# Optimization experiments

Hardware: AMD Instinct MI355X
Metric: run time of the kernel (lower is better)

## Reference

```python
import jax, jax.numpy as jnp
import numpy as np

B, L, D, H, I = 4, 1024, 2048, 16, 8192
DH = D // H  # 128
EPS = 1e-6


def setup_inputs() -> dict:
    key = jax.random.key(0)
    ks = jax.random.split(key, 10)
    hidden_states = jax.random.normal(ks[0], (B, L, D), dtype=jnp.float32)
    # additive causal mask [B,1,L,L]: 0 on allowed, large negative on masked
    causal = jnp.tril(jnp.ones((L, L), dtype=bool))
    attention_mask = jnp.where(causal, 0.0, -1e9).astype(jnp.float32)
    attention_mask = jnp.broadcast_to(attention_mask[None, None], (B, 1, L, L))
    # RoPE tables [B,L,DH]
    inv_freq = 1.0 / (10000.0 ** (jnp.arange(0, DH, 2, dtype=jnp.float32) / DH))
    pos = jnp.arange(L, dtype=jnp.float32)
    freqs = pos[:, None] * inv_freq[None, :]            # [L, DH/2]
    emb = jnp.concatenate([freqs, freqs], axis=-1)       # [L, DH]
    cos = jnp.broadcast_to(jnp.cos(emb)[None], (B, L, DH)).astype(jnp.float32)
    sin = jnp.broadcast_to(jnp.sin(emb)[None], (B, L, DH)).astype(jnp.float32)
    s = 0.02
    return {
        "hidden_states": hidden_states,
        "attention_mask": attention_mask,
        "cos": cos,
        "sin": sin,
        "q_w": jax.random.normal(ks[1], (D, D), jnp.float32) * s,
        "k_w": jax.random.normal(ks[2], (D, D), jnp.float32) * s,
        "v_w": jax.random.normal(ks[3], (D, D), jnp.float32) * s,
        "o_w": jax.random.normal(ks[4], (D, D), jnp.float32) * s,
        "gate_w": jax.random.normal(ks[5], (I, D), jnp.float32) * s,
        "up_w": jax.random.normal(ks[6], (I, D), jnp.float32) * s,
        "down_w": jax.random.normal(ks[7], (D, I), jnp.float32) * s,
        "ln1_w": jnp.ones((D,), jnp.float32),
        "ln2_w": jnp.ones((D,), jnp.float32),
    }


def _rms_norm(x, w):
    var = jnp.mean(jnp.square(x), axis=-1, keepdims=True)
    return x * jax.lax.rsqrt(var + EPS) * w


def _rotate_half(x):
    x1, x2 = jnp.split(x, 2, axis=-1)
    return jnp.concatenate([-x2, x1], axis=-1)


def reference(hidden_states, attention_mask, cos, sin, q_w, k_w, v_w, o_w,
              gate_w, up_w, down_w, ln1_w, ln2_w):
    residual = hidden_states
    h = _rms_norm(hidden_states, ln1_w)                       # [B,L,D]
    # QKV projections (torch Linear: x @ W^T)
    def heads(x, w):
        return (x @ w.T).reshape(B, L, H, DH).transpose(0, 2, 1, 3)  # [B,H,L,DH]
    q, k, v = heads(h, q_w), heads(h, k_w), heads(h, v_w)
    cos_b, sin_b = cos[:, None], sin[:, None]                 # [B,1,L,DH]
    q = q * cos_b + _rotate_half(q) * sin_b
    k = k * cos_b + _rotate_half(k) * sin_b
    scores = jnp.einsum('bhqd,bhkd->bhqk', q, k) / jnp.sqrt(jnp.float32(DH))
    scores = scores + attention_mask                          # [B,H,L,L]
    attn = jax.nn.softmax(scores, axis=-1)
    ctx = jnp.einsum('bhqk,bhkd->bhqd', attn, v)              # [B,H,L,DH]
    ctx = ctx.transpose(0, 2, 1, 3).reshape(B, L, D)
    attn_out = ctx @ o_w.T
    h1 = residual + attn_out
    h2 = _rms_norm(h1, ln2_w)
    mlp = (jax.nn.silu(h2 @ gate_w.T) * (h2 @ up_w.T)) @ down_w.T
    out = h1 + mlp
    return out, attn
```

## Files before the change

kernel.cpp:

```cpp
#include <hip/hip_runtime.h>


typedef __bf16 bf16;
typedef __bf16 bf16x8 __attribute__((ext_vector_type(8)));
typedef __bf16 bf16x4 __attribute__((ext_vector_type(4)));
typedef float  f32x4  __attribute__((ext_vector_type(4)));

constexpr int   kB  = 4;
constexpr int   kL  = 1024;
constexpr int   kD  = 2048;
constexpr int   kH  = 16;
constexpr int   kI  = 8192;
constexpr int   kDH = 128;
constexpr int   kQKV = 3 * kD;
constexpr float kEps = 1e-6f;
constexpr float kScoreScale = 0.08838834764831845f;

typedef __attribute__((address_space(1))) void gvoid_t;
typedef __attribute__((address_space(3))) void lvoid_t;

__device__ __forceinline__ void gload_lds16(const void* g, void* l) {
  __builtin_amdgcn_global_load_lds((gvoid_t*)g, (lvoid_t*)l, 16, 0, 0);
}

#define ASM_VMCNT(n) asm volatile("s_waitcnt vmcnt(" #n ")" ::: "memory")

__device__ __forceinline__ void bar_raw() {
  asm volatile("" ::: "memory");
  __builtin_amdgcn_s_barrier();
  asm volatile("" ::: "memory");
}

__global__ __launch_bounds__(256) void cast_f32_bf16_kernel(
    const float* __restrict__ x, bf16* __restrict__ y, long n) {
  long i = ((long)blockIdx.x * 256 + threadIdx.x) * 4;
  long stride = (long)gridDim.x * 256 * 4;
  for (; i < n; i += stride) {
    const float4 v = *reinterpret_cast<const float4*>(x + i);
    bf16x4 o;
    o[0] = (bf16)v.x; o[1] = (bf16)v.y; o[2] = (bf16)v.z; o[3] = (bf16)v.w;
    *reinterpret_cast<bf16x4*>(y + i) = o;
  }
}

__global__ __launch_bounds__(256) void rmsnorm_kernel(
    const float* __restrict__ x, const float* __restrict__ w,
    bf16* __restrict__ out) {
  const long row = blockIdx.x;
  const float* xr = x + row * (long)kD;
  bf16* orow = out + row * (long)kD;
  const int t = threadIdx.x;

  float4 v0 = *(const float4*)(xr + t * 8);
  float4 v1 = *(const float4*)(xr + t * 8 + 4);
  float ss = v0.x * v0.x + v0.y * v0.y + v0.z * v0.z + v0.w * v0.w +
             v1.x * v1.x + v1.y * v1.y + v1.z * v1.z + v1.w * v1.w;

  __shared__ float red[4];
  for (int off = 32; off > 0; off >>= 1) ss += __shfl_down(ss, off);
  if ((t & 63) == 0) red[t >> 6] = ss;
  __syncthreads();
  const float tot = red[0] + red[1] + red[2] + red[3];
  const float rs = rsqrtf(tot / (float)kD + kEps);

  float4 w0 = *(const float4*)(w + t * 8);
  float4 w1 = *(const float4*)(w + t * 8 + 4);
  bf16x8 o;
  o[0] = (bf16)(v0.x * rs * w0.x); o[1] = (bf16)(v0.y * rs * w0.y);
  o[2] = (bf16)(v0.z * rs * w0.z); o[3] = (bf16)(v0.w * rs * w0.w);
  o[4] = (bf16)(v1.x * rs * w1.x); o[5] = (bf16)(v1.y * rs * w1.y);
  o[6] = (bf16)(v1.z * rs * w1.z); o[7] = (bf16)(v1.w * rs * w1.w);
  *(bf16x8*)(orow + t * 8) = o;
}

__global__ __launch_bounds__(256) void rope_kernel(
    bf16* __restrict__ qkv, const float* __restrict__ cosb,
    const float* __restrict__ sinb) {
  const long row = blockIdx.x;
  const float* cr = cosb + row * (long)kDH;
  const float* sr = sinb + row * (long)kDH;
  bf16* qr = qkv + row * (long)kQKV;
  bf16* kr = qr + kD;
  const int t = threadIdx.x;
#pragma unroll
  for (int it = 0; it < 4; ++it) {
    const int p = it * 256 + t;
    const int h = p >> 6, i = p & 63;
    const int i0 = h * kDH + i, i1 = i0 + 64;
    const float c0 = cr[i], s0 = sr[i], c1 = cr[i + 64], s1 = sr[i + 64];
    const float q0 = (float)qr[i0], q1 = (float)qr[i1];
    qr[i0] = (bf16)(q0 * c0 - q1 * s0);
    qr[i1] = (bf16)(q1 * c1 + q0 * s1);
    const float k0 = (float)kr[i0], k1 = (float)kr[i1];
    kr[i0] = (bf16)(k0 * c0 - k1 * s0);
    kr[i1] = (bf16)(k1 * c1 + k0 * s1);
  }
}

__global__ __launch_bounds__(256) void transpose_v_kernel(
    const bf16* __restrict__ qkv, bf16* __restrict__ vT) {
  __shared__ bf16 tile[32][33];
  const int z = blockIdx.z, b = z / kH, h = z % kH;
  const bf16* src = qkv + (long)b * kL * kQKV + 2 * kD + h * kDH;
  bf16* dst = vT + (long)z * kDH * kL;
  const int l0 = blockIdx.x * 32, d0 = blockIdx.y * 32;
  const int tx = threadIdx.x & 31, ty = threadIdx.x >> 5;
  for (int r = ty; r < 32; r += 8)
    tile[r][tx] = src[(long)(l0 + r) * kQKV + d0 + tx];
  __syncthreads();
  for (int r = ty; r < 32; r += 8)
    dst[(long)(d0 + r) * kL + l0 + tx] = tile[tx][r];
}

__global__ __launch_bounds__(256) void merge_stats_kernel(
    const float2* __restrict__ sp, float2* __restrict__ sm) {
  const int idx = blockIdx.x * 256 + threadIdx.x;
  const int row = idx & 1023;
  const int n = ((row >> 7) + 1) * 2;
  const float2* p = sp + ((long)idx << 4);
  float M = -3.0e38f;
  for (int i = 0; i < n; ++i) M = fmaxf(M, p[i].x);
  float S = 0.f;
  for (int i = 0; i < n; ++i) S += p[i].y * expf(p[i].x - M);
  sm[idx] = make_float2(M, 1.0f / S);
}

enum { EPI_NONE = 0, EPI_ADD = 1, EPI_SILU = 3, EPI_OUTADD = 4,
       EPI_PASS1 = 6, EPI_PASS2 = 7 };

template <typename OutT, int EPI, bool AF32, int NF, bool CK>
__device__ __forceinline__ void gemm_body(
    const void* __restrict__ Ap, long sAo, long sAi, int lda,
    const bf16* __restrict__ Bp, long sBo, long sBi, int ldb,
    OutT* Cp, long sCo, long sCi, int ldc,
    const void* Ep, long sEo, long sEi, int lde,
    float scale, int Hdiv, int M, int N, int K) {
  constexpr int BN = 32 * NF;
  constexpr int ACH = 512;
  constexpr int BCH = BN * 4;
  static_assert((EPI != EPI_PASS1 && EPI != EPI_PASS2) || NF == 4, "pass NF=4");

  const int z = blockIdx.z;
  const int zo = z / Hdiv, zi = z % Hdiv;

  const bf16* A = nullptr;
  const float* Af = nullptr;
  if constexpr (AF32) Af = (const float*)Ap + zo * sAo + zi * sAi;
  else                A  = (const bf16*)Ap + zo * sAo + zi * sAi;
  const bf16* Bw = Bp + zo * sBo + zi * sBi;
  OutT* C = Cp + zo * sCo + zi * sCi;

  const int t = threadIdx.x;
  const int m0 = blockIdx.y * 128, n0 = blockIdx.x * BN;

  if constexpr (EPI == EPI_PASS1) {
    if (blockIdx.x > blockIdx.y) return;
  }
  if constexpr (EPI == EPI_PASS2) {
    if (blockIdx.x > blockIdx.y) {
      for (int e = t; e < 128 * 32; e += 256) {
        const int row = e >> 5, col = (e & 31) * 4;
        *(float4*)&C[(long)(m0 + row) * ldc + n0 + col] =
            make_float4(0.f, 0.f, 0.f, 0.f);
      }
      return;
    }
  }

  __shared__ __align__(16) bf16 lsA[2][128 * 32];
  __shared__ __align__(16) bf16 lsB[2][BN * 32];

  const int wave = t >> 6, lane = t & 63;
  const int wm = (wave >> 1) * 64, wn = (wave & 1) * (NF * 16);
  const int lr = lane & 15, lg = lane >> 4;

  f32x4 acc[4][NF] = {};

  auto stage = [&](int buf, int k0) {
    if constexpr (AF32) {
#pragma unroll
      for (int c = 0; c < 2; ++c) {
        const int id = c * 256 + t;
        const int row = id >> 2, col = (id & 3) * 8;
        const float* src = Af + (long)(m0 + row) * lda + k0 + col;
        const float4 u0 = *(const float4*)src;
        const float4 u1 = *(const float4*)(src + 4);
        bf16x8 wv;
        wv[0] = (bf16)u0.x; wv[1] = (bf16)u0.y; wv[2] = (bf16)u0.z; wv[3] = (bf16)u0.w;
        wv[4] = (bf16)u1.x; wv[5] = (bf16)u1.y; wv[6] = (bf16)u1.z; wv[7] = (bf16)u1.w;
        *(bf16x8*)&lsA[buf][id * 8] = wv;
        if (NF == 4 || c == 0)
          gload_lds16(Bw + (long)(n0 + row) * ldb + k0 + col, &lsB[buf][id * 8]);
      }
    } else {
#pragma unroll
      for (int c = 0; c < (ACH + BCH) / 256; ++c) {
        const int id = c * 256 + t;
        if (id < ACH) {
          const int row = id >> 2, col = (id & 3) * 8;
          gload_lds16(A + (long)(m0 + row) * lda + k0 + col, &lsA[buf][id * 8]);
        } else {
          const int fid = id - ACH;
          const int row = fid >> 2, col = (fid & 3) * 8;
          gload_lds16(Bw + (long)(n0 + row) * ldb + k0 + col, &lsB[buf][fid * 8]);
        }
      }
    }
  };

  auto compute = [&](int buf) {
    bf16x8 af[4], bfr[NF];
#pragma unroll
    for (int i = 0; i < 4; ++i)
      af[i] = *(const bf16x8*)&lsA[buf][(wm + i * 16 + lr) * 32 + lg * 8];
#pragma unroll
    for (int j = 0; j < NF; ++j)
      bfr[j] = *(const bf16x8*)&lsB[buf][(wn + j * 16 + lr) * 32 + lg * 8];
#pragma unroll
    for (int i = 0; i < 4; ++i)
#pragma unroll
      for (int j = 0; j < NF; ++j)
        acc[i][j] = __builtin_amdgcn_mfma_f32_16x16x32_bf16(af[i], bfr[j],
                                                            acc[i][j], 0, 0, 0);
  };

  const int Klim = CK ? (m0 + 128) : K;
  int cur = 0;

  if constexpr (AF32) {
    stage(0, 0);
    __syncthreads();
    for (int k0 = 0; k0 < Klim - 32; k0 += 32) {
      stage(cur ^ 1, k0 + 32);
      compute(cur);
      __syncthreads();
      cur ^= 1;
    }
    compute(cur);
  } else {
    stage(0, 0);
    for (int k0 = 0; k0 < Klim - 32; k0 += 32) {
      stage(cur ^ 1, k0 + 32);
      if constexpr (NF == 4) ASM_VMCNT(4); else ASM_VMCNT(3);
      bar_raw();
      compute(cur);
      bar_raw();
      cur ^= 1;
    }
    ASM_VMCNT(0);
    bar_raw();
    compute(cur);
  }

  if constexpr (EPI == EPI_PASS1) {
    float2* statsP = (float2*)Ep;
    const int half = wn >> 6, nt = blockIdx.x;
#pragma unroll
    for (int i = 0; i < 4; ++i) {
#pragma unroll
      for (int r = 0; r < 4; ++r) {
        const int rowg = m0 + wm + i * 16 + lg * 4 + r;
        float v[NF];
        float mx = -3.0e38f;
#pragma unroll
        for (int j = 0; j < NF; ++j) {
          const int colg = n0 + wn + j * 16 + lr;
          v[j] = acc[i][j][r] * scale + (colg > rowg ? -1.0e9f : 0.0f);
          mx = fmaxf(mx, v[j]);
        }
        for (int sh = 1; sh <= 8; sh <<= 1) mx = fmaxf(mx, __shfl_xor(mx, sh));
        float s = 0.f;
#pragma unroll
        for (int j = 0; j < NF; ++j) s += expf(v[j] - mx);
        for (int sh = 1; sh <= 8; sh <<= 1) s += __shfl_xor(s, sh);
        if (lr == 0)
          statsP[(((long)(z << 10) + rowg) << 4) + nt * 2 + half] =
              make_float2(mx, s);
      }
    }
  } else if constexpr (EPI == EPI_PASS2) {
    const float2* sm = (const float2*)Ep;
#pragma unroll
    for (int i = 0; i < 4; ++i) {
#pragma unroll
      for (int j = 0; j < NF; ++j) {
        const int colg = n0 + wn + j * 16 + lr;
#pragma unroll
        for (int r = 0; r < 4; ++r) {
          const int rowg = m0 + wm + i * 16 + lg * 4 + r;
          float p = 0.0f;
          if (colg <= rowg) {
            const float2 st = sm[(z << 10) + rowg];
            p = expf(acc[i][j][r] * scale - st.x) * st.y;
          }
          C[(long)rowg * ldc + colg] = (OutT)p;
        }
      }
    }
  } else {
    const float* Ef = (const float*)Ep;
    const bf16* Eb = (const bf16*)Ep;
    long ebase = 0;
    if constexpr (EPI == EPI_ADD || EPI == EPI_SILU)
      ebase = zo * sEo + zi * sEi;
#pragma unroll
    for (int i = 0; i < 4; ++i) {
#pragma unroll
      for (int j = 0; j < NF; ++j) {
        const int col = n0 + wn + j * 16 + lr;
#pragma unroll
        for (int r = 0; r < 4; ++r) {
          const int rowi = m0 + wm + i * 16 + lg * 4 + r;
          float val = acc[i][j][r] * scale;
          const long idx = (long)rowi * ldc + col;
          if constexpr (EPI == EPI_ADD)
            val += Ef[ebase + (long)rowi * lde + col];
          if constexpr (EPI == EPI_SILU) {
            const float g = (float)Eb[ebase + (long)rowi * lde + col];
            val = (g / (1.0f + expf(-g))) * val;
          }
          if constexpr (EPI == EPI_OUTADD)
            val += (float)C[idx];
          C[idx] = (OutT)val;
        }
      }
    }
  }
}

#define GEMM_ARGS                                                        \
  const void* __restrict__ Ap, long sAo, long sAi, int lda,              \
  const bf16* __restrict__ Bp, long sBo, long sBi, int ldb,              \
  void* Cp, long sCo, long sCi, int ldc,                                 \
  const void* Ep, long sEo, long sEi, int lde,                           \
  float scale, int Hdiv, int M, int N, int K
#define GEMM_PASS Ap, sAo, sAi, lda, Bp, sBo, sBi, ldb, (OUT_T*)Cp, sCo, \
  sCi, ldc, Ep, sEo, sEi, lde, scale, Hdiv, M, N, K

#define DEF_GEMM(NAME, OUT_TY, EPI_V, AF32_V, NF_V, CK_V)                \
  __global__ __launch_bounds__(256) void NAME(GEMM_ARGS) {               \
    using OUT_T = OUT_TY;                                                \
    gemm_body<OUT_T, EPI_V, AF32_V, NF_V, CK_V>(GEMM_PASS);              \
  }

DEF_GEMM(gemm_qkv,   bf16,  EPI_NONE,   false, 4, false)
DEF_GEMM(gemm_sc1,   float, EPI_PASS1,  false, 4, false)
DEF_GEMM(gemm_sc2,   float, EPI_PASS2,  false, 4, false)
DEF_GEMM(gemm_ctx,   bf16,  EPI_NONE,   true,  2, true)
DEF_GEMM(gemm_oproj, float, EPI_ADD,    false, 2, false)
DEF_GEMM(gemm_gate,  bf16,  EPI_NONE,   false, 4, false)
DEF_GEMM(gemm_up,    bf16,  EPI_SILU,   false, 4, false)
DEF_GEMM(gemm_down,  float, EPI_OUTADD, false, 2, false)

extern "C" void kernel_launch(void* const* d_in, const int* in_sizes, int n_in,
                              void* d_out, int out_size, void* d_ws,
                              size_t ws_size, hipStream_t stream) {
  (void)in_sizes; (void)n_in; (void)out_size; (void)ws_size;

  const float* hidden = (const float*)d_in[0];
  const float* cosb   = (const float*)d_in[2];
  const float* sinb   = (const float*)d_in[3];
  const float* q_w    = (const float*)d_in[4];
  const float* k_w    = (const float*)d_in[5];
  const float* v_w    = (const float*)d_in[6];
  const float* o_w    = (const float*)d_in[7];
  const float* gate_w = (const float*)d_in[8];
  const float* up_w   = (const float*)d_in[9];
  const float* down_w = (const float*)d_in[10];
  const float* ln1    = (const float*)d_in[11];
  const float* ln2    = (const float*)d_in[12];

  float* out  = (float*)d_out;
  float* attn = out + (long)kB * kL * kD;

  bf16* wsb = (bf16*)d_ws;
  long off = 0;
  bf16* WQKV = wsb + off; off += 3L * kD * kD;
  bf16* WO   = wsb + off; off += (long)kD * kD;
  bf16* WBIG = wsb + off; off += (long)kI * kD;
  bf16* HBF  = wsb + off; off += (long)kB * kL * kD;
  bf16* QKV  = wsb + off; off += (long)kB * kL * kQKV;
  bf16* GBUF = wsb + off; off += (long)kB * kL * kI;

  float2* STATS_P = (float2*)HBF;
  float2* STATS_M = STATS_P + (64L * 1024 * 16);

  const long DD = (long)kD * kD;
  const long ID = (long)kI * kD;
  const int  ML = kB * kL;

  cast_f32_bf16_kernel<<<dim3((int)(DD / 1024)), 256, 0, stream>>>(q_w, WQKV, DD);
  cast_f32_bf16_kernel<<<dim3((int)(DD / 1024)), 256, 0, stream>>>(k_w, WQKV + DD, DD);
  cast_f32_bf16_kernel<<<dim3((int)(DD / 1024)), 256, 0, stream>>>(v_w, WQKV + 2 * DD, DD);
  cast_f32_bf16_kernel<<<dim3((int)(DD / 1024)), 256, 0, stream>>>(o_w, WO, DD);

  rmsnorm_kernel<<<ML, 256, 0, stream>>>(hidden, ln1, HBF);

  gemm_qkv<<<dim3(kQKV / 128, ML / 128, 1), 256, 0, stream>>>(
      HBF, 0, 0, kD, WQKV, 0, 0, kD, QKV, 0, 0, kQKV,
      nullptr, 0, 0, 0, 1.0f, 1, ML, kQKV, kD);

  rope_kernel<<<ML, 256, 0, stream>>>(QKV, cosb, sinb);

  transpose_v_kernel<<<dim3(kL / 32, kDH / 32, kB * kH), 256, 0, stream>>>(QKV, GBUF);

  gemm_sc1<<<dim3(kL / 128, kL / 128, kB * kH), 256, 0, stream>>>(
      QKV, (long)kL * kQKV, kDH, kQKV,
      QKV + kD, (long)kL * kQKV, kDH, kQKV,
      attn, (long)kH * kL * kL, (long)kL * kL, kL,
      STATS_P, 0, 0, 0,
      kScoreScale, kH, kL, kL, kDH);

  merge_stats_kernel<<<256, 256, 0, stream>>>(STATS_P, STATS_M);

  gemm_sc2<<<dim3(kL / 128, kL / 128, kB * kH), 256, 0, stream>>>(
      QKV, (long)kL * kQKV, kDH, kQKV,
      QKV + kD, (long)kL * kQKV, kDH, kQKV,
      attn, (long)kH * kL * kL, (long)kL * kL, kL,
      STATS_M, 0, 0, 0,
      kScoreScale, kH, kL, kL, kDH);

  gemm_ctx<<<dim3(kDH / 64, kL / 128, kB * kH), 256, 0, stream>>>(
      attn, (long)kH * kL * kL, (long)kL * kL, kL,
      GBUF, (long)kH * kDH * kL, (long)kDH * kL, kL,
      HBF, (long)kL * kD, kDH, kD,
      nullptr, 0, 0, 0, 1.0f, kH, kL, kDH, kL);

  gemm_oproj<<<dim3(kD / 64, ML / 128, 1), 256, 0, stream>>>(
      HBF, 0, 0, kD, WO, 0, 0, kD, out, 0, 0, kD,
      hidden, 0, 0, kD, 1.0f, 1, ML, kD, kD);

  bf16* H2 = QKV;
  rmsnorm_kernel<<<ML, 256, 0, stream>>>(out, ln2, H2);

  cast_f32_bf16_kernel<<<dim3((int)(ID / 1024)), 256, 0, stream>>>(gate_w, WBIG, ID);
  gemm_gate<<<dim3(kI / 128, ML / 128, 1), 256, 0, stream>>>(
      H2, 0, 0, kD, WBIG, 0, 0, kD, GBUF, 0, 0, kI,
      nullptr, 0, 0, 0, 1.0f, 1, ML, kI, kD);

  cast_f32_bf16_kernel<<<dim3((int)(ID / 1024)), 256, 0, stream>>>(up_w, WBIG, ID);
  gemm_up<<<dim3(kI / 128, ML / 128, 1), 256, 0, stream>>>(
      H2, 0, 0, kD, WBIG, 0, 0, kD, GBUF, 0, 0, kI,
      GBUF, 0, 0, kI, 1.0f, 1, ML, kI, kD);

  cast_f32_bf16_kernel<<<dim3((int)(ID / 1024)), 256, 0, stream>>>(down_w, WBIG, ID);
  gemm_down<<<dim3(kD / 64, ML / 128, 1), 256, 0, stream>>>(
      GBUF, 0, 0, kI, WBIG, 0, 0, kI, out, 0, 0, kD,
      nullptr, 0, 0, 0, 1.0f, 1, ML, kD, kI);
}
```

Baseline: 1.153 ms.

## Fuse gate/up GEMMs with SiLU, add XCD block swizzle, simplify pipeline sync

Replaces the separate gate and up GEMMs (gate writes bf16 to GBUF, up rereads it for the SiLU epilogue) with one gemm_mlp kernel. It loads the activation tile once, computes both gate and up accumulators, and applies SiLU*up in registers, removing an intermediate round trip. It also adds an XCD-aware block index remap for the qkv, oproj and down GEMMs to improve L2 locality. Separately, it drops the hand-tuned vmcnt/raw-barrier pipeline for bf16 inputs in favour of plain __syncthreads, which may reduce load/compute overlap. It needs an extra 8192x2048 bf16 weight buffer in workspace.

```diff
diff --git a/kernel.cpp b/kernel.cpp
--- a/kernel.cpp
+++ b/kernel.cpp
@@ -21,14 +21,6 @@
 
 __device__ __forceinline__ void gload_lds16(const void* g, void* l) {
   __builtin_amdgcn_global_load_lds((gvoid_t*)g, (lvoid_t*)l, 16, 0, 0);
-}
-
-#define ASM_VMCNT(n) asm volatile("s_waitcnt vmcnt(" #n ")" ::: "memory")
-
-__device__ __forceinline__ void bar_raw() {
-  asm volatile("" ::: "memory");
-  __builtin_amdgcn_s_barrier();
-  asm volatile("" ::: "memory");
 }
 
 __global__ __launch_bounds__(256) void cast_f32_bf16_kernel(
@@ -125,10 +117,9 @@
   sm[idx] = make_float2(M, 1.0f / S);
 }
 
-enum { EPI_NONE = 0, EPI_ADD = 1, EPI_SILU = 3, EPI_OUTADD = 4,
-       EPI_PASS1 = 6, EPI_PASS2 = 7 };
-
-template <typename OutT, int EPI, bool AF32, int NF, bool CK>
+enum { EPI_NONE = 0, EPI_ADD = 1, EPI_OUTADD = 4, EPI_PASS1 = 6, EPI_PASS2 = 7 };
+
+template <typename OutT, int EPI, bool AF32, int NF, bool CK, bool SWZ>
 __device__ __forceinline__ void gemm_body(
     const void* __restrict__ Ap, long sAo, long sAi, int lda,
     const bf16* __restrict__ Bp, long sBo, long sBi, int ldb,
@@ -151,7 +142,16 @@
   OutT* C = Cp + zo * sCo + zi * sCi;
 
   const int t = threadIdx.x;
-  const int m0 = blockIdx.y * 128, n0 = blockIdx.x * BN;
+
+  int bx = blockIdx.x, by = blockIdx.y;
+  if constexpr (SWZ) {
+    const int nn = gridDim.x, nm = gridDim.y;
+    const int f = by * nn + bx;
+    const int xcd = f & 7, j = f >> 3;
+    by = j % nm;
+    bx = xcd * (nn >> 3) + j / nm;
+  }
+  const int m0 = by * 128, n0 = bx * BN;
 
   if constexpr (EPI == EPI_PASS1) {
     if (blockIdx.x > blockIdx.y) return;
@@ -225,32 +225,17 @@
   };
 
   const int Klim = CK ? (m0 + 128) : K;
+
+  stage(0, 0);
+  __syncthreads();
   int cur = 0;
-
-  if constexpr (AF32) {
-    stage(0, 0);
+  for (int k0 = 0; k0 < Klim - 32; k0 += 32) {
+    stage(cur ^ 1, k0 + 32);
+    compute(cur);
     __syncthreads();
-    for (int k0 = 0; k0 < Klim - 32; k0 += 32) {
-      stage(cur ^ 1, k0 + 32);
-      compute(cur);
-      __syncthreads();
-      cur ^= 1;
-    }
-    compute(cur);
-  } else {
-    stage(0, 0);
-    for (int k0 = 0; k0 < Klim - 32; k0 += 32) {
-      stage(cur ^ 1, k0 + 32);
-      if constexpr (NF == 4) ASM_VMCNT(4); else ASM_VMCNT(3);
-      bar_raw();
-      compute(cur);
-      bar_raw();
-      cur ^= 1;
-    }
-    ASM_VMCNT(0);
-    bar_raw();
-    compute(cur);
-  }
+    cur ^= 1;
+  }
+  compute(cur);
 
   if constexpr (EPI == EPI_PASS1) {
     float2* statsP = (float2*)Ep;
@@ -299,9 +284,8 @@
     }
   } else {
     const float* Ef = (const float*)Ep;
-    const bf16* Eb = (const bf16*)Ep;
     long ebase = 0;
-    if constexpr (EPI == EPI_ADD || EPI == EPI_SILU)
+    if constexpr (EPI == EPI_ADD)
       ebase = zo * sEo + zi * sEi;
 #pragma unroll
     for (int i = 0; i < 4; ++i) {
@@ -315,10 +299,6 @@
           const long idx = (long)rowi * ldc + col;
           if constexpr (EPI == EPI_ADD)
             val += Ef[ebase + (long)rowi * lde + col];
-          if constexpr (EPI == EPI_SILU) {
-            const float g = (float)Eb[ebase + (long)rowi * lde + col];
-            val = (g / (1.0f + expf(-g))) * val;
-          }
           if constexpr (EPI == EPI_OUTADD)
             val += (float)C[idx];
           C[idx] = (OutT)val;
@@ -337,20 +317,99 @@
 #define GEMM_PASS Ap, sAo, sAi, lda, Bp, sBo, sBi, ldb, (OUT_T*)Cp, sCo, \
   sCi, ldc, Ep, sEo, sEi, lde, scale, Hdiv, M, N, K
 
-#define DEF_GEMM(NAME, OUT_TY, EPI_V, AF32_V, NF_V, CK_V)                \
+#define DEF_GEMM(NAME, OUT_TY, EPI_V, AF32_V, NF_V, CK_V, SWZ_V)         \
   __global__ __launch_bounds__(256) void NAME(GEMM_ARGS) {               \
     using OUT_T = OUT_TY;                                                \
-    gemm_body<OUT_T, EPI_V, AF32_V, NF_V, CK_V>(GEMM_PASS);              \
-  }
-
-DEF_GEMM(gemm_qkv,   bf16,  EPI_NONE,   false, 4, false)
-DEF_GEMM(gemm_sc1,   float, EPI_PASS1,  false, 4, false)
-DEF_GEMM(gemm_sc2,   float, EPI_PASS2,  false, 4, false)
-DEF_GEMM(gemm_ctx,   bf16,  EPI_NONE,   true,  2, true)
-DEF_GEMM(gemm_oproj, float, EPI_ADD,    false, 2, false)
-DEF_GEMM(gemm_gate,  bf16,  EPI_NONE,   false, 4, false)
-DEF_GEMM(gemm_up,    bf16,  EPI_SILU,   false, 4, false)
-DEF_GEMM(gemm_down,  float, EPI_OUTADD, false, 2, false)
+    gemm_body<OUT_T, EPI_V, AF32_V, NF_V, CK_V, SWZ_V>(GEMM_PASS);       \
+  }
+
+DEF_GEMM(gemm_qkv,   bf16,  EPI_NONE,   false, 4, false, true)
+DEF_GEMM(gemm_sc1,   float, EPI_PASS1,  false, 4, false, false)
+DEF_GEMM(gemm_sc2,   float, EPI_PASS2,  false, 4, false, false)
+DEF_GEMM(gemm_ctx,   bf16,  EPI_NONE,   true,  2, true,  false)
+DEF_GEMM(gemm_oproj, float, EPI_ADD,    false, 2, false, true)
+DEF_GEMM(gemm_down,  float, EPI_OUTADD, false, 2, false, true)
+
+__global__ __launch_bounds__(256) void gemm_mlp(
+    const bf16* __restrict__ A, const bf16* __restrict__ Bg,
+    const bf16* __restrict__ Bu, bf16* __restrict__ C) {
+  const int t = threadIdx.x;
+  const int nn = gridDim.x, nm = gridDim.y;
+  const int f = blockIdx.y * nn + blockIdx.x;
+  const int xcd = f & 7, j = f >> 3;
+  const int m0 = (j % nm) * 128;
+  const int n0 = (xcd * (nn >> 3) + j / nm) * 64;
+
+  __shared__ __align__(16) bf16 lsA[2][128 * 32];
+  __shared__ __align__(16) bf16 lsG[2][64 * 32];
+  __shared__ __align__(16) bf16 lsU[2][64 * 32];
+
+  const int wave = t >> 6, lane = t & 63;
+  const int wm = (wave >> 1) * 64, wn = (wave & 1) * 32;
+  const int lr = lane & 15, lg = lane >> 4;
+
+  f32x4 ag[4][2] = {}, au[4][2] = {};
+
+  auto stage = [&](int buf, int k0) {
+#pragma unroll
+    for (int c = 0; c < 2; ++c) {
+      const int id = c * 256 + t;
+      const int row = id >> 2, col = (id & 3) * 8;
+      gload_lds16(A + (long)(m0 + row) * kD + k0 + col, &lsA[buf][id * 8]);
+    }
+    {
+      const int row = t >> 2, col = (t & 3) * 8;
+      gload_lds16(Bg + (long)(n0 + row) * kD + k0 + col, &lsG[buf][t * 8]);
+      gload_lds16(Bu + (long)(n0 + row) * kD + k0 + col, &lsU[buf][t * 8]);
+    }
+  };
+
+  auto compute = [&](int buf) {
+    bf16x8 af[4], bg[2], bu[2];
+#pragma unroll
+    for (int i = 0; i < 4; ++i)
+      af[i] = *(const bf16x8*)&lsA[buf][(wm + i * 16 + lr) * 32 + lg * 8];
+#pragma unroll
+    for (int jj = 0; jj < 2; ++jj) {
+      bg[jj] = *(const bf16x8*)&lsG[buf][(wn + jj * 16 + lr) * 32 + lg * 8];
+      bu[jj] = *(const bf16x8*)&lsU[buf][(wn + jj * 16 + lr) * 32 + lg * 8];
+    }
+#pragma unroll
+    for (int i = 0; i < 4; ++i)
+#pragma unroll
+      for (int jj = 0; jj < 2; ++jj) {
+        ag[i][jj] = __builtin_amdgcn_mfma_f32_16x16x32_bf16(af[i], bg[jj],
+                                                            ag[i][jj], 0, 0, 0);
+        au[i][jj] = __builtin_amdgcn_mfma_f32_16x16x32_bf16(af[i], bu[jj],
+                                                            au[i][jj], 0, 0, 0);
+      }
+  };
+
+  stage(0, 0);
+  __syncthreads();
+  int cur = 0;
+  for (int k0 = 0; k0 < kD - 32; k0 += 32) {
+    stage(cur ^ 1, k0 + 32);
+    compute(cur);
+    __syncthreads();
+    cur ^= 1;
+  }
+  compute(cur);
+
+#pragma unroll
+  for (int i = 0; i < 4; ++i) {
+#pragma unroll
+    for (int jj = 0; jj < 2; ++jj) {
+      const int col = n0 + wn + jj * 16 + lr;
+#pragma unroll
+      for (int r = 0; r < 4; ++r) {
+        const int row = m0 + wm + i * 16 + lg * 4 + r;
+        const float g = ag[i][jj][r], u = au[i][jj][r];
+        C[(long)row * kI + col] = (bf16)((g / (1.0f + expf(-g))) * u);
+      }
+    }
+  }
+}
 
 extern "C" void kernel_launch(void* const* d_in, const int* in_sizes, int n_in,
                               void* d_out, int out_size, void* d_ws,
@@ -377,7 +436,8 @@
   long off = 0;
   bf16* WQKV = wsb + off; off += 3L * kD * kD;
   bf16* WO   = wsb + off; off += (long)kD * kD;
-  bf16* WBIG = wsb + off; off += (long)kI * kD;
+  bf16* WG   = wsb + off; off += (long)kI * kD;
+  bf16* WU   = wsb + off; off += (long)kI * kD;
   bf16* HBF  = wsb + off; off += (long)kB * kL * kD;
   bf16* QKV  = wsb + off; off += (long)kB * kL * kQKV;
   bf16* GBUF = wsb + off; off += (long)kB * kL * kI;
@@ -433,18 +493,12 @@
   bf16* H2 = QKV;
   rmsnorm_kernel<<<ML, 256, 0, stream>>>(out, ln2, H2);
 
-  cast_f32_bf16_kernel<<<dim3((int)(ID / 1024)), 256, 0, stream>>>(gate_w, WBIG, ID);
-  gemm_gate<<<dim3(kI / 128, ML / 128, 1), 256, 0, stream>>>(
-      H2, 0, 0, kD, WBIG, 0, 0, kD, GBUF, 0, 0, kI,
-      nullptr, 0, 0, 0, 1.0f, 1, ML, kI, kD);
-
-  cast_f32_bf16_kernel<<<dim3((int)(ID / 1024)), 256, 0, stream>>>(up_w, WBIG, ID);
-  gemm_up<<<dim3(kI / 128, ML / 128, 1), 256, 0, stream>>>(
-      H2, 0, 0, kD, WBIG, 0, 0, kD, GBUF, 0, 0, kI,
-      GBUF, 0, 0, kI, 1.0f, 1, ML, kI, kD);
-
-  cast_f32_bf16_kernel<<<dim3((int)(ID / 1024)), 256, 0, stream>>>(down_w, WBIG, ID);
+  cast_f32_bf16_kernel<<<dim3((int)(ID / 1024)), 256, 0, stream>>>(gate_w, WG, ID);
+  cast_f32_bf16_kernel<<<dim3((int)(ID / 1024)), 256, 0, stream>>>(up_w, WU, ID);
+  gemm_mlp<<<dim3(kI / 64, ML / 128, 1), 256, 0, stream>>>(H2, WG, WU, GBUF);
+
+  cast_f32_bf16_kernel<<<dim3((int)(ID / 1024)), 256, 0, stream>>>(down_w, WU, ID);
   gemm_down<<<dim3(kD / 64, ML / 128, 1), 256, 0, stream>>>(
-      GBUF, 0, 0, kI, WBIG, 0, 0, kI, out, 0, 0, kD,
+      GBUF, 0, 0, kI, WU, 0, 0, kI, out, 0, 0, kD,
       nullptr, 0, 0, 0, 1.0f, 1, ML, kD, kI);
 }
```

Result: slower. 1.353 ms (+17.3%).
